# Performance work log

Hardware: AMD Instinct MI355X
Metric: run time of the kernel (lower is better)

## Reference

```python
import jax, jax.numpy as jnp
import numpy as np

D = 256   # embedding dim d; rows are d+1 = 257
N = 2048  # sequence length n; cols are n+1 = 2049
B = 16

def setup_inputs() -> dict:
    key = jax.random.key(0)
    k_h, k_p, k_q = jax.random.split(key, 3)
    H = jax.random.normal(k_h, (B, D + 1, N + 1), dtype=jnp.float32)
    P = jax.random.normal(k_p, (D + 1, D + 1), dtype=jnp.float32) * 0.01
    Q = jax.random.normal(k_q, (D + 1, D + 1), dtype=jnp.float32) * 0.01
    return {"H": H, "P": P, "Q": Q}

def reference(H, P, Q):
    # H: (B, d+1, n+1)
    n = H.shape[2] - 1
    # HtQH = H^T @ Q @ H : (B, n+1, n+1)
    HtQ = jnp.einsum('bds,de->bse', H, Q)          # (B, n+1, d+1)
    HtQH = jnp.einsum('bse,bet->bst', HtQ, H)      # (B, n+1, n+1)
    # mask M = diag(1,...,1,0): M @ HtQH zeroes the last row
    MHtQH = HtQH.at[:, -1, :].set(0.0)
    PH = jnp.einsum('de,bet->bdt', P, H)           # (B, d+1, n+1)
    attn = jnp.einsum('bds,bst->bdt', PH, MHtQH)   # (B, d+1, n+1)
    return H + attn / n
```

## Files before the change

kernel.cpp:

```cpp
#include <hip/hip_runtime.h>
#include <hip/hip_bf16.h>

#define DP    257
#define NP    2049
#define NSEQ  2048
#define NB    16
#define KLD   288
#define HROWS 320
#define TROWS 2304
#define KPAD  40

typedef __attribute__((ext_vector_type(8))) short bf16x8;
typedef __attribute__((ext_vector_type(4))) short bf16x4;
typedef __attribute__((ext_vector_type(4))) float f32x4;

__global__ __launch_bounds__(256) void conv_h(const float* __restrict__ H,
                                              __hip_bfloat16* __restrict__ Hb,
                                              __hip_bfloat16* __restrict__ Hbt) {
    const int b  = blockIdx.z;
    const int t0 = blockIdx.x * 64;
    const int e0 = blockIdx.y * 64;
    const float* __restrict__ Hs = H + (size_t)b * DP * NP;
    __hip_bfloat16* __restrict__ Hbb  = Hb  + (size_t)b * HROWS * 2048;
    __hip_bfloat16* __restrict__ Hbtb = Hbt + (size_t)b * TROWS * KLD;

    __shared__ float tile[64][65];

    const int tl = threadIdx.x & 63;
    const int er = threadIdx.x >> 6;
#pragma unroll
    for (int r = 0; r < 16; ++r) {
        const int el = er + r * 4;
        const int ge = e0 + el;
        const int gt = t0 + tl;
        float v = 0.f;
        if (ge < DP && gt < NP) v = Hs[(size_t)ge * NP + gt];
        tile[el][tl] = v;
        if (ge < HROWS && gt < 2048) Hbb[(size_t)ge * 2048 + gt] = __float2bfloat16(v);
    }
    __syncthreads();
#pragma unroll
    for (int r = 0; r < 16; ++r) {
        const int ttl = er + r * 4;
        const int gt = t0 + ttl;
        const int ge = e0 + tl;
        if (gt < TROWS && ge < KLD)
            Hbtb[(size_t)gt * KLD + ge] = __float2bfloat16(tile[tl][ttl]);
    }
}

__global__ __launch_bounds__(256) void conv_pq(const float* __restrict__ P,
                                               const float* __restrict__ Q,
                                               __hip_bfloat16* __restrict__ Pb,
                                               __hip_bfloat16* __restrict__ Qt) {
    const int c0 = blockIdx.x * 64;
    const int r0 = blockIdx.y * 64;
    const int tl = threadIdx.x & 63;
    const int rr = threadIdx.x >> 6;
    __shared__ float tile[64][65];

    if (blockIdx.z == 0) {
#pragma unroll
        for (int r = 0; r < 16; ++r) {
            const int m = r0 + rr + r * 4;
            const int k = c0 + tl;
            float v = (m < DP && k < DP) ? P[m * DP + k] : 0.f;
            if (m < KLD && k < KLD) Pb[m * KLD + k] = __float2bfloat16(v);
        }
    } else {
#pragma unroll
        for (int r = 0; r < 16; ++r) {
            const int k = r0 + rr + r * 4;
            const int n = c0 + tl;
            float v = (k < DP && n < DP) ? Q[k * DP + n] : 0.f;
            tile[k - r0][n - c0] = v;
        }
        __syncthreads();
#pragma unroll
        for (int r = 0; r < 16; ++r) {
            const int k = r0 + tl;
            const int n = c0 + rr + r * 4;
            if (n < KLD && k < KLD) Qt[n * KLD + k] = __float2bfloat16(tile[tl][n - c0]);
        }
    }
}

__global__ __launch_bounds__(512, 4) void gram_staged(const __hip_bfloat16* __restrict__ Hb,
                                                      __hip_bfloat16* __restrict__ G) {
    const int b  = blockIdx.y;
    const int tm = blockIdx.x / 5;
    const int tn = blockIdx.x % 5;
    const int m0 = tm * 64, n0 = tn * 64;
    const int tid = threadIdx.x;
    const int wave = tid >> 6, lane = tid & 63;
    const int lrow = lane & 15, kq = (lane >> 4) * 8;
    const int hw = wave >> 2;
    const int q  = wave & 3;
    const int mh = (q & 1) * 32, nh = (q >> 1) * 32;
    const int hs = tid >> 8;
    const int t2 = tid & 255;
    const int sr = t2 >> 2;
    const int sc = (t2 & 3) * 8;

    __shared__ __align__(16) char smem[2 * 2 * 2 * 64 * KPAD * 2];
    short* As = (short*)smem;
    short* Bs = (short*)(smem + 2 * 2 * 64 * KPAD * 2);
    float* red = (float*)smem;

    const short* __restrict__ base = (const short*)(Hb + (size_t)b * HROWS * 2048);

    auto aoff = [&](int buf, int h, int r) { return ((buf * 2 + h) * 64 + r) * KPAD; };

    f32x4 acc[2][2] = {};

    {
        const int kb = hs * 1024;
        *(bf16x8*)&As[aoff(0, hs, sr) + sc] = *(const bf16x8*)(base + (size_t)(m0 + sr) * 2048 + kb + sc);
        *(bf16x8*)&Bs[aoff(0, hs, sr) + sc] = *(const bf16x8*)(base + (size_t)(n0 + sr) * 2048 + kb + sc);
    }
    __syncthreads();

    for (int kt = 0; kt < 32; ++kt) {
        const int cur = kt & 1, nxt = cur ^ 1;
        if (kt + 1 < 32) {
            const int kb = hs * 1024 + (kt + 1) * 32;
            *(bf16x8*)&As[aoff(nxt, hs, sr) + sc] = *(const bf16x8*)(base + (size_t)(m0 + sr) * 2048 + kb + sc);
            *(bf16x8*)&Bs[aoff(nxt, hs, sr) + sc] = *(const bf16x8*)(base + (size_t)(n0 + sr) * 2048 + kb + sc);
        }
        bf16x8 a0 = *(const bf16x8*)&As[aoff(cur, hw, mh + lrow) + kq];
        bf16x8 a1 = *(const bf16x8*)&As[aoff(cur, hw, mh + 16 + lrow) + kq];
        bf16x8 b0 = *(const bf16x8*)&Bs[aoff(cur, hw, nh + lrow) + kq];
        bf16x8 b1 = *(const bf16x8*)&Bs[aoff(cur, hw, nh + 16 + lrow) + kq];
        acc[0][0] = __builtin_amdgcn_mfma_f32_16x16x32_bf16(a0, b0, acc[0][0], 0, 0, 0);
        acc[0][1] = __builtin_amdgcn_mfma_f32_16x16x32_bf16(a0, b1, acc[0][1], 0, 0, 0);
        acc[1][0] = __builtin_amdgcn_mfma_f32_16x16x32_bf16(a1, b0, acc[1][0], 0, 0, 0);
        acc[1][1] = __builtin_amdgcn_mfma_f32_16x16x32_bf16(a1, b1, acc[1][1], 0, 0, 0);
        __syncthreads();
    }

    const int ccol  = lane & 15;
    const int crow0 = (lane >> 4) * 4;
#pragma unroll
    for (int i = 0; i < 2; ++i)
#pragma unroll
        for (int j = 0; j < 2; ++j)
#pragma unroll
            for (int r = 0; r < 4; ++r)
                red[((wave * 32) + i * 16 + crow0 + r) * 32 + j * 16 + ccol] = acc[i][j][r];
    __syncthreads();

    const int q2  = tid >> 7;
    const int t7  = tid & 127;
    const int row = t7 >> 2;
    const int c8  = (t7 & 3) * 8;
    const int gm = m0 + (q2 & 1) * 32 + row;
    const int gn = n0 + (q2 >> 1) * 32 + c8;
    if (gm < KLD && gn < KLD) {
        __hip_bfloat16 o[8];
#pragma unroll
        for (int t = 0; t < 8; ++t) {
            const float v = red[((q2 * 32) + row) * 32 + c8 + t] +
                            red[(((q2 + 4) * 32) + row) * 32 + c8 + t];
            o[t] = __float2bfloat16((gm < DP && (gn + t) < DP) ? v : 0.f);
        }
        __hip_bfloat16* __restrict__ Gb = G + (size_t)b * KLD * KLD;
        *(bf16x8*)&Gb[gm * KLD + gn] = *(const bf16x8*)o;
    }
}

__global__ __launch_bounds__(256) void mm_sk4(const __hip_bfloat16* __restrict__ A,
                                              const __hip_bfloat16* __restrict__ B,
                                              __hip_bfloat16* __restrict__ C,
                                              int strideA, int strideB) {
    const int b  = blockIdx.y;
    const int tm = blockIdx.x / 9;
    const int tn = blockIdx.x % 9;
    const int s    = threadIdx.x >> 6;
    const int lane = threadIdx.x & 63;
    const int lrow = lane & 15;
    const int koff = (lane >> 4) * 8;
    const short* __restrict__ Ab = (const short*)(A + (size_t)b * strideA);
    const short* __restrict__ Bb = (const short*)(B + (size_t)b * strideB);
    const int m0 = tm * 32, n0 = tn * 32;

    __shared__ float red[4][32][32];

    f32x4 acc[2][2] = {};
    for (int kt = s; kt < 9; kt += 4) {
        const int k0 = kt * 32;
        bf16x8 a0 = *(const bf16x8*)(Ab + (m0 + lrow)      * KLD + k0 + koff);
        bf16x8 a1 = *(const bf16x8*)(Ab + (m0 + 16 + lrow) * KLD + k0 + koff);
        bf16x8 c0 = *(const bf16x8*)(Bb + (n0 + lrow)      * KLD + k0 + koff);
        bf16x8 c1 = *(const bf16x8*)(Bb + (n0 + 16 + lrow) * KLD + k0 + koff);
        acc[0][0] = __builtin_amdgcn_mfma_f32_16x16x32_bf16(a0, c0, acc[0][0], 0, 0, 0);
        acc[0][1] = __builtin_amdgcn_mfma_f32_16x16x32_bf16(a0, c1, acc[0][1], 0, 0, 0);
        acc[1][0] = __builtin_amdgcn_mfma_f32_16x16x32_bf16(a1, c0, acc[1][0], 0, 0, 0);
        acc[1][1] = __builtin_amdgcn_mfma_f32_16x16x32_bf16(a1, c1, acc[1][1], 0, 0, 0);
    }

    const int ccol  = lane & 15;
    const int crow0 = (lane >> 4) * 4;
#pragma unroll
    for (int i = 0; i < 2; ++i)
#pragma unroll
        for (int j = 0; j < 2; ++j)
#pragma unroll
            for (int r = 0; r < 4; ++r)
                red[s][i * 16 + crow0 + r][j * 16 + ccol] = acc[i][j][r];
    __syncthreads();

    const int row = threadIdx.x >> 3;
    const int c4  = (threadIdx.x & 7) * 4;
    float4 v0 = *(const float4*)&red[0][row][c4];
    float4 v1 = *(const float4*)&red[1][row][c4];
    float4 v2 = *(const float4*)&red[2][row][c4];
    float4 v3 = *(const float4*)&red[3][row][c4];
    float sum[4] = {v0.x + v1.x + v2.x + v3.x,
                    v0.y + v1.y + v2.y + v3.y,
                    v0.z + v1.z + v2.z + v3.z,
                    v0.w + v1.w + v2.w + v3.w};
    const int gm = m0 + row;
    const int gn = n0 + c4;
    __hip_bfloat16 o[4];
#pragma unroll
    for (int t = 0; t < 4; ++t) {
        const float v = (gm < DP && (gn + t) < DP) ? sum[t] : 0.f;
        o[t] = __float2bfloat16(v);
    }
    __hip_bfloat16* __restrict__ Cb = C + (size_t)b * KLD * KLD;
    *(bf16x4*)&Cb[gm * KLD + gn] = *(const bf16x4*)o;
}

__global__ __launch_bounds__(256, 3) void attn_staged(const __hip_bfloat16* __restrict__ Kb,
                                                      const __hip_bfloat16* __restrict__ Hbt,
                                                      const float* __restrict__ H,
                                                      float* __restrict__ Out) {
    const int b  = blockIdx.z;
    const int d0 = blockIdx.y * 64;
    const int t0 = blockIdx.x * 256;
    const int tid = threadIdx.x;
    const int wave = tid >> 6, lane = tid & 63;
    const int lrow = lane & 15, kq = (lane >> 4) * 8;
    const int sr = tid >> 2;
    const int sc = (tid & 3) * 8;

    __shared__ __align__(16) short As[2][64][KPAD];
    __shared__ __align__(16) short Bs[2][256][KPAD];

    const short* __restrict__ Ka = (const short*)(Kb  + (size_t)b * KLD * KLD);
    const short* __restrict__ Ta = (const short*)(Hbt + (size_t)b * TROWS * KLD);

    int rA = d0 + sr; if (rA > KLD - 1) rA = KLD - 1;

    f32x4 acc[4][4] = {};

    *(bf16x8*)&As[0][sr][sc] = *(const bf16x8*)(Ka + (size_t)rA * KLD + sc);
#pragma unroll
    for (int c = 0; c < 4; ++c)
        *(bf16x8*)&Bs[0][sr + 64 * c][sc] = *(const bf16x8*)(Ta + (size_t)(t0 + sr + 64 * c) * KLD + sc);
    __syncthreads();

    for (int kt = 0; kt < 9; ++kt) {
        const int cur = kt & 1, nxt = cur ^ 1;
        if (kt + 1 < 9) {
            const int e0 = (kt + 1) * 32;
            *(bf16x8*)&As[nxt][sr][sc] = *(const bf16x8*)(Ka + (size_t)rA * KLD + e0 + sc);
#pragma unroll
            for (int c = 0; c < 4; ++c)
                *(bf16x8*)&Bs[nxt][sr + 64 * c][sc] = *(const bf16x8*)(Ta + (size_t)(t0 + sr + 64 * c) * KLD + e0 + sc);
        }
        bf16x8 af[4], bfr[4];
#pragma unroll
        for (int i = 0; i < 4; ++i) af[i]  = *(const bf16x8*)&As[cur][i * 16 + lrow][kq];
#pragma unroll
        for (int j = 0; j < 4; ++j) bfr[j] = *(const bf16x8*)&Bs[cur][wave * 64 + j * 16 + lrow][kq];
#pragma unroll
        for (int i = 0; i < 4; ++i)
#pragma unroll
            for (int j = 0; j < 4; ++j)
                acc[i][j] = __builtin_amdgcn_mfma_f32_16x16x32_bf16(af[i], bfr[j], acc[i][j], 0, 0, 0);
        __syncthreads();
    }

    const float* __restrict__ Hs = H + (size_t)b * DP * NP;
    float* __restrict__ Ob = Out + (size_t)b * DP * NP;
    const float inv_n = 1.0f / (float)NSEQ;
    const int ccol  = lane & 15;
    const int crow0 = (lane >> 4) * 4;
#pragma unroll
    for (int i = 0; i < 4; ++i)
#pragma unroll
        for (int j = 0; j < 4; ++j)
#pragma unroll
            for (int r = 0; r < 4; ++r) {
                const int gd = d0 + i * 16 + crow0 + r;
                const int gt = t0 + wave * 64 + j * 16 + ccol;
                if (gd < DP && gt < NP) {
                    const size_t idx = (size_t)gd * NP + gt;
                    Ob[idx] = Hs[idx] + inv_n * acc[i][j][r];
                }
            }
}

extern "C" void kernel_launch(void* const* d_in, const int* in_sizes, int n_in,
                              void* d_out, int out_size, void* d_ws, size_t ws_size,
                              hipStream_t stream) {
    const float* H = (const float*)d_in[0];
    const float* P = (const float*)d_in[1];
    const float* Q = (const float*)d_in[2];
    float* out = (float*)d_out;

    __hip_bfloat16* Hb  = (__hip_bfloat16*)d_ws;
    __hip_bfloat16* Hbt = Hb  + (size_t)NB * HROWS * 2048;
    __hip_bfloat16* G   = Hbt + (size_t)NB * TROWS * KLD;
    __hip_bfloat16* Pb  = G   + (size_t)NB * KLD * KLD;
    __hip_bfloat16* Qt  = Pb  + (size_t)KLD * KLD;
    __hip_bfloat16* W   = Hb;
    __hip_bfloat16* Kb  = Hb + (size_t)NB * KLD * KLD;

    conv_pq<<<dim3(5, 5, 2),   256, 0, stream>>>(P, Q, Pb, Qt);
    conv_h <<<dim3(36, 5, NB), 256, 0, stream>>>(H, Hb, Hbt);
    gram_staged<<<dim3(25, NB), 512, 0, stream>>>(Hb, G);
    mm_sk4<<<dim3(81, NB), 256, 0, stream>>>(Pb, G, W, 0, KLD * KLD);
    mm_sk4<<<dim3(81, NB), 256, 0, stream>>>(W, Qt, Kb, KLD * KLD, 0);
    attn_staged<<<dim3(9, 5, NB), 256, 0, stream>>>(Kb, Hbt, H, out);
}
```

Measured before the change: 194.8 us.

## Shrink attention tiles, register-prefetch single-buffered LDS, coalesce epilogue via LDS staging

The final attention GEMM kernel now uses 64x128 tiles instead of 64x256, with a 2x2 wave split and grid 17x5 instead of 9x5. It targets occupancy 4, prefetches the next K-slice into registers, and uses a single LDS buffer with an extra barrier. The epilogue stages accumulators through LDS so rows are written with coalesced stores. The transposed H buffer gets a 320 pitch and fewer padded rows, which trims conversion work, but the extra barriers and smaller tiles give less reuse per block.

```diff
diff --git a/kernel.cpp b/kernel.cpp
--- a/kernel.cpp
+++ b/kernel.cpp
@@ -1,14 +1,15 @@
 #include <hip/hip_runtime.h>
 #include <hip/hip_bf16.h>
 
-#define DP    257
-#define NP    2049
-#define NSEQ  2048
-#define NB    16
-#define KLD   288
-#define HROWS 320
-#define TROWS 2304
-#define KPAD  40
+#define DP     257
+#define NP     2049
+#define NSEQ   2048
+#define NB     16
+#define KLD    288
+#define HROWS  320
+#define TPITCH 320
+#define TROWS  2176
+#define KPAD   40
 
 typedef __attribute__((ext_vector_type(8))) short bf16x8;
 typedef __attribute__((ext_vector_type(4))) short bf16x4;
@@ -22,7 +23,7 @@
     const int e0 = blockIdx.y * 64;
     const float* __restrict__ Hs = H + (size_t)b * DP * NP;
     __hip_bfloat16* __restrict__ Hbb  = Hb  + (size_t)b * HROWS * 2048;
-    __hip_bfloat16* __restrict__ Hbtb = Hbt + (size_t)b * TROWS * KLD;
+    __hip_bfloat16* __restrict__ Hbtb = Hbt + (size_t)b * TROWS * TPITCH;
 
     __shared__ float tile[64][65];
 
@@ -44,8 +45,10 @@
         const int ttl = er + r * 4;
         const int gt = t0 + ttl;
         const int ge = e0 + tl;
-        if (gt < TROWS && ge < KLD)
-            Hbtb[(size_t)gt * KLD + ge] = __float2bfloat16(tile[tl][ttl]);
+        if (gt < TROWS && ge < TPITCH) {
+            const float v = (ge < KLD) ? tile[tl][ttl] : 0.f;
+            Hbtb[(size_t)gt * TPITCH + ge] = __float2bfloat16(v);
+        }
     }
 }
 
@@ -231,55 +234,66 @@
     *(bf16x4*)&Cb[gm * KLD + gn] = *(const bf16x4*)o;
 }
 
-__global__ __launch_bounds__(256, 3) void attn_staged(const __hip_bfloat16* __restrict__ Kb,
-                                                      const __hip_bfloat16* __restrict__ Hbt,
-                                                      const float* __restrict__ H,
-                                                      float* __restrict__ Out) {
+__global__ __launch_bounds__(256, 4) void attn_v2(const __hip_bfloat16* __restrict__ Kb,
+                                                  const __hip_bfloat16* __restrict__ Hbt,
+                                                  const float* __restrict__ H,
+                                                  float* __restrict__ Out) {
     const int b  = blockIdx.z;
     const int d0 = blockIdx.y * 64;
-    const int t0 = blockIdx.x * 256;
+    const int t0 = blockIdx.x * 128;
     const int tid = threadIdx.x;
     const int wave = tid >> 6, lane = tid & 63;
     const int lrow = lane & 15, kq = (lane >> 4) * 8;
+    const int dh = (wave & 1) * 32;
+    const int th = (wave >> 1) * 64;
     const int sr = tid >> 2;
     const int sc = (tid & 3) * 8;
 
-    __shared__ __align__(16) short As[2][64][KPAD];
-    __shared__ __align__(16) short Bs[2][256][KPAD];
+    __shared__ __align__(16) char smem[(64 + 128) * KPAD * 2];
+    short* As = (short*)smem;
+    short* Bs = (short*)(smem + 64 * KPAD * 2);
+    float* Ped = (float*)smem;
 
     const short* __restrict__ Ka = (const short*)(Kb  + (size_t)b * KLD * KLD);
-    const short* __restrict__ Ta = (const short*)(Hbt + (size_t)b * TROWS * KLD);
+    const short* __restrict__ Ta = (const short*)(Hbt + (size_t)b * TROWS * TPITCH);
 
     int rA = d0 + sr; if (rA > KLD - 1) rA = KLD - 1;
 
-    f32x4 acc[4][4] = {};
-
-    *(bf16x8*)&As[0][sr][sc] = *(const bf16x8*)(Ka + (size_t)rA * KLD + sc);
-#pragma unroll
-    for (int c = 0; c < 4; ++c)
-        *(bf16x8*)&Bs[0][sr + 64 * c][sc] = *(const bf16x8*)(Ta + (size_t)(t0 + sr + 64 * c) * KLD + sc);
+    f32x4 acc[2][4] = {};
+
+    bf16x8 pA  = *(const bf16x8*)(Ka + (size_t)rA * KLD + sc);
+    bf16x8 pB0 = *(const bf16x8*)(Ta + (size_t)(t0 + sr) * TPITCH + sc);
+    bf16x8 pB1 = *(const bf16x8*)(Ta + (size_t)(t0 + 64 + sr) * TPITCH + sc);
+    *(bf16x8*)&As[sr * KPAD + sc]        = pA;
+    *(bf16x8*)&Bs[sr * KPAD + sc]        = pB0;
+    *(bf16x8*)&Bs[(64 + sr) * KPAD + sc] = pB1;
     __syncthreads();
 
     for (int kt = 0; kt < 9; ++kt) {
-        const int cur = kt & 1, nxt = cur ^ 1;
-        if (kt + 1 < 9) {
+        if (kt < 8) {
             const int e0 = (kt + 1) * 32;
-            *(bf16x8*)&As[nxt][sr][sc] = *(const bf16x8*)(Ka + (size_t)rA * KLD + e0 + sc);
-#pragma unroll
-            for (int c = 0; c < 4; ++c)
-                *(bf16x8*)&Bs[nxt][sr + 64 * c][sc] = *(const bf16x8*)(Ta + (size_t)(t0 + sr + 64 * c) * KLD + e0 + sc);
-        }
-        bf16x8 af[4], bfr[4];
-#pragma unroll
-        for (int i = 0; i < 4; ++i) af[i]  = *(const bf16x8*)&As[cur][i * 16 + lrow][kq];
-#pragma unroll
-        for (int j = 0; j < 4; ++j) bfr[j] = *(const bf16x8*)&Bs[cur][wave * 64 + j * 16 + lrow][kq];
-#pragma unroll
-        for (int i = 0; i < 4; ++i)
-#pragma unroll
-            for (int j = 0; j < 4; ++j)
-                acc[i][j] = __builtin_amdgcn_mfma_f32_16x16x32_bf16(af[i], bfr[j], acc[i][j], 0, 0, 0);
-        __syncthreads();
+            pA  = *(const bf16x8*)(Ka + (size_t)rA * KLD + e0 + sc);
+            pB0 = *(const bf16x8*)(Ta + (size_t)(t0 + sr) * TPITCH + e0 + sc);
+            pB1 = *(const bf16x8*)(Ta + (size_t)(t0 + 64 + sr) * TPITCH + e0 + sc);
+        }
+        bf16x8 af0 = *(const bf16x8*)&As[(dh + lrow) * KPAD + kq];
+        bf16x8 af1 = *(const bf16x8*)&As[(dh + 16 + lrow) * KPAD + kq];
+        bf16x8 bfr[4];
+#pragma unroll
+        for (int j = 0; j < 4; ++j)
+            bfr[j] = *(const bf16x8*)&Bs[(th + j * 16 + lrow) * KPAD + kq];
+#pragma unroll
+        for (int j = 0; j < 4; ++j) {
+            acc[0][j] = __builtin_amdgcn_mfma_f32_16x16x32_bf16(af0, bfr[j], acc[0][j], 0, 0, 0);
+            acc[1][j] = __builtin_amdgcn_mfma_f32_16x16x32_bf16(af1, bfr[j], acc[1][j], 0, 0, 0);
+        }
+        __syncthreads();
+        if (kt < 8) {
+            *(bf16x8*)&As[sr * KPAD + sc]        = pA;
+            *(bf16x8*)&Bs[sr * KPAD + sc]        = pB0;
+            *(bf16x8*)&Bs[(64 + sr) * KPAD + sc] = pB1;
+            __syncthreads();
+        }
     }
 
     const float* __restrict__ Hs = H + (size_t)b * DP * NP;
@@ -287,19 +301,38 @@
     const float inv_n = 1.0f / (float)NSEQ;
     const int ccol  = lane & 15;
     const int crow0 = (lane >> 4) * 4;
-#pragma unroll
-    for (int i = 0; i < 4; ++i)
-#pragma unroll
-        for (int j = 0; j < 4; ++j)
-#pragma unroll
-            for (int r = 0; r < 4; ++r) {
-                const int gd = d0 + i * 16 + crow0 + r;
-                const int gt = t0 + wave * 64 + j * 16 + ccol;
-                if (gd < DP && gt < NP) {
-                    const size_t idx = (size_t)gd * NP + gt;
-                    Ob[idx] = Hs[idx] + inv_n * acc[i][j][r];
+
+#pragma unroll
+    for (int c = 0; c < 4; ++c) {
+        if ((wave & 1) == (c >> 1)) {
+            const int i = c & 1;
+#pragma unroll
+            for (int j = 0; j < 4; ++j)
+#pragma unroll
+                for (int r = 0; r < 4; ++r)
+                    Ped[(crow0 + r) * 132 + th + j * 16 + ccol] = acc[i][j][r];
+        }
+        __syncthreads();
+#pragma unroll
+        for (int p = 0; p < 2; ++p) {
+            const int row = (tid >> 5) + p * 8;
+            const int col = (tid & 31) * 4;
+            const int gd = d0 + c * 16 + row;
+            if (gd < DP) {
+                const float* src = &Ped[row * 132 + col];
+                const size_t base = (size_t)gd * NP;
+#pragma unroll
+                for (int cc = 0; cc < 4; ++cc) {
+                    const int gt = t0 + col + cc;
+                    if (gt < NP) {
+                        const size_t idx = base + gt;
+                        Ob[idx] = Hs[idx] + inv_n * src[cc];
+                    }
                 }
             }
+        }
+        __syncthreads();
+    }
 }
 
 extern "C" void kernel_launch(void* const* d_in, const int* in_sizes, int n_in,
@@ -312,16 +345,16 @@
 
     __hip_bfloat16* Hb  = (__hip_bfloat16*)d_ws;
     __hip_bfloat16* Hbt = Hb  + (size_t)NB * HROWS * 2048;
-    __hip_bfloat16* G   = Hbt + (size_t)NB * TROWS * KLD;
+    __hip_bfloat16* G   = Hbt + (size_t)NB * TROWS * TPITCH;
     __hip_bfloat16* Pb  = G   + (size_t)NB * KLD * KLD;
     __hip_bfloat16* Qt  = Pb  + (size_t)KLD * KLD;
     __hip_bfloat16* W   = Hb;
     __hip_bfloat16* Kb  = Hb + (size_t)NB * KLD * KLD;
 
     conv_pq<<<dim3(5, 5, 2),   256, 0, stream>>>(P, Q, Pb, Qt);
-    conv_h <<<dim3(36, 5, NB), 256, 0, stream>>>(H, Hb, Hbt);
+    conv_h <<<dim3(34, 5, NB), 256, 0, stream>>>(H, Hb, Hbt);
     gram_staged<<<dim3(25, NB), 512, 0, stream>>>(Hb, G);
     mm_sk4<<<dim3(81, NB), 256, 0, stream>>>(Pb, G, W, 0, KLD * KLD);
     mm_sk4<<<dim3(81, NB), 256, 0, stream>>>(W, Qt, Kb, KLD * KLD, 0);
-    attn_staged<<<dim3(9, 5, NB), 256, 0, stream>>>(Kb, Hbt, H, out);
-}
+    attn_v2<<<dim3(17, 5, NB), 256, 0, stream>>>(Kb, Hbt, H, out);
+}
```

Result: no change. 192.0 us (-1.5%).
